# Kernel tuning notes

Hardware: AMD Instinct MI355X
Metric: run time of the kernel (lower is better)

## Reference

```python
import jax, jax.numpy as jnp
import numpy as np

B, C_IN, L = 16, 64, 1024
HID, OUT, ORDER = 1024, 512, 4
EPS = 1e-5


def setup_inputs() -> dict:
    key = jax.random.key(0)
    ks = jax.random.split(key, 4)
    return {
        "x": jax.random.normal(ks[0], (B, C_IN, L), jnp.float32),
        "W_in": jax.random.normal(ks[1], (C_IN, HID), jnp.float32) / np.sqrt(C_IN).astype(np.float32),
        "b_in": jnp.zeros((HID,), jnp.float32),
        "coeffs1": jax.random.normal(ks[2], (HID, HID, ORDER), jnp.float32) * 0.01,
        "bias1": jnp.zeros((HID,), jnp.float32),
        "g1": jnp.ones((HID,), jnp.float32),
        "beta1": jnp.zeros((HID,), jnp.float32),
        "coeffs2": jax.random.normal(ks[3], (OUT, HID, ORDER), jnp.float32) * 0.01,
        "bias2": jnp.zeros((OUT,), jnp.float32),
        "g2": jnp.ones((OUT,), jnp.float32),
        "beta2": jnp.zeros((OUT,), jnp.float32),
    }


def _taylor_kan(x, coeffs, bias):
    # x: (B, L, C_in); coeffs: (out, C_in, order); y[b,l,o] = sum_i sum_c x^i * coeffs[o,c,i]
    # Expressed as order-wise GEMMs with a running power -- no (B,out,L,C) expand.
    order = coeffs.shape[-1]
    y = jnp.zeros(x.shape[:2] + (coeffs.shape[0],), x.dtype)
    xp = jnp.ones_like(x)  # x**0 (matches torch 0**0 == 1)
    for i in range(order):
        y = y + jnp.einsum('blc,oc->blo', xp, coeffs[:, :, i])
        if i + 1 < order:
            xp = xp * x
    return y + bias


def _layernorm(x, g, b):
    mu = jnp.mean(x, -1, keepdims=True)
    var = jnp.mean((x - mu) ** 2, -1, keepdims=True)
    return (x - mu) * jax.lax.rsqrt(var + EPS) * g + b


def reference(x, W_in, b_in, coeffs1, bias1, g1, beta1, coeffs2, bias2, g2, beta2):
    # x: (B, C_in, L) -> project channels to hidden: (B, L, HID)
    h = jnp.einsum('bcl,ch->blh', x, W_in) + b_in
    h = _taylor_kan(h, coeffs1, bias1)            # (B, L, HID)
    h = jax.nn.gelu(_layernorm(h, g1, beta1), approximate=False)
    h = _taylor_kan(h, coeffs2, bias2)            # (B, L, OUT)
    h = _layernorm(h, g2, beta2)
    return jnp.mean(h, axis=1)                    # adaptive avg pool over L -> (B, OUT)
```

## Files before the change

### kernel.cpp

```cpp
#include <hip/hip_runtime.h>
#include <math.h>

#define Bsz  16
#define CIN  64
#define LEN  1024
#define HIDN 1024
#define OUTN 512
#define MTOT (Bsz*LEN)
#define KTOT (3*HIDN)
#define LCHUNKS 32
#define LROWS   (LEN/LCHUNKS)

typedef __attribute__((ext_vector_type(8))) short bf16x8;
typedef __attribute__((ext_vector_type(16))) float f32x16;

__device__ __forceinline__ unsigned short f2bf(float x) {
    union { float f; unsigned int u; } v; v.f = x;
    unsigned int r = v.u + 0x7fff + ((v.u >> 16) & 1);
    return (unsigned short)(r >> 16);
}
__device__ __forceinline__ float bf2f(unsigned short u) {
    union { unsigned int u; float f; } v; v.u = ((unsigned int)u) << 16;
    return v.f;
}
__device__ __forceinline__ void gload_lds16(const void* g, void* l) {
    __builtin_amdgcn_global_load_lds((const __attribute__((address_space(1))) void*)g,
                                     (__attribute__((address_space(3))) void*)l, 16, 0, 0);
}

__global__ __launch_bounds__(256) void prep_all(const float* __restrict__ coeffs1,
                                                const float* __restrict__ bias1,
                                                const float* __restrict__ coeffs2,
                                                const float* __restrict__ bias2,
                                                const float* __restrict__ x,
                                                const float* __restrict__ Win,
                                                unsigned short* __restrict__ W1T,
                                                float* __restrict__ b1e,
                                                unsigned short* __restrict__ W2T,
                                                float* __restrict__ b2e,
                                                unsigned short* __restrict__ xT,
                                                unsigned short* __restrict__ WinT) {
    __shared__ float sm[64 * 65];
    int bid = blockIdx.x, t = threadIdx.x;
    if (bid < 1536) {
        const float* coeffs; const float* bias; unsigned short* WT; float* beff; int o;
        if (bid < 1024) { coeffs = coeffs1; bias = bias1; WT = W1T; beff = b1e; o = bid; }
        else            { coeffs = coeffs2; bias = bias2; WT = W2T; beff = b2e; o = bid - 1024; }
        float s = 0.f;
        unsigned short* wrow = WT + (size_t)o * KTOT;
        for (int c = t; c < HIDN; c += 256) {
            float4 v = *(const float4*)(coeffs + ((size_t)o * HIDN + c) * 4);
            s += v.x;
            wrow[c]            = f2bf(v.y);
            wrow[HIDN + c]     = f2bf(v.z);
            wrow[2 * HIDN + c] = f2bf(v.w);
        }
        for (int off = 32; off > 0; off >>= 1) s += __shfl_down(s, off, 64);
        if ((t & 63) == 0) sm[t >> 6] = s;
        __syncthreads();
        if (t == 0) beff[o] = bias[o] + sm[0] + sm[1] + sm[2] + sm[3];
    } else {
        const float* src; unsigned short* dstbase; size_t src_rstride;
        int c0;
        if (bid < 1792) {
            int tile = bid - 1536; int b = tile >> 4; c0 = (tile & 15) * 64;
            src = x + (size_t)b * CIN * LEN;  src_rstride = LEN;
            dstbase = xT + ((size_t)b * LEN + c0) * CIN;
        } else {
            int tile = bid - 1792; c0 = tile * 64;
            src = Win; src_rstride = HIDN;
            dstbase = WinT + (size_t)c0 * CIN;
        }
#pragma unroll
        for (int it = 0; it < 4; it++) {
            int idx = t + it * 256;
            int c = idx >> 4, q = idx & 15;
            float4 v = *(const float4*)(src + (size_t)c * src_rstride + c0 + q * 4);
            sm[c * 65 + q * 4 + 0] = v.x;
            sm[c * 65 + q * 4 + 1] = v.y;
            sm[c * 65 + q * 4 + 2] = v.z;
            sm[c * 65 + q * 4 + 3] = v.w;
        }
        __syncthreads();
        int ll = t >> 2, cg = (t & 3) * 16;
        unsigned short* dst = dstbase + (size_t)ll * CIN + cg;
#pragma unroll
        for (int j = 0; j < 4; j++) {
            int c = cg + j * 4;
            ushort4 w = { f2bf(sm[(c + 0) * 65 + ll]), f2bf(sm[(c + 1) * 65 + ll]),
                          f2bf(sm[(c + 2) * 65 + ll]), f2bf(sm[(c + 3) * 65 + ll]) };
            *(ushort4*)(dst + j * 4) = w;
        }
    }
}

__global__ __launch_bounds__(256) void proj_mfma(const unsigned short* __restrict__ xT,
                                                 const unsigned short* __restrict__ WinT,
                                                 const float* __restrict__ bin,
                                                 unsigned short* __restrict__ Hpow) {
    __shared__ unsigned short As[128 * 64];
    __shared__ unsigned short Bs[128 * 64];
    int t = threadIdx.x, lane = t & 63, wave = t >> 6;
    int m0 = blockIdx.x * 128, n0 = blockIdx.y * 128;
    int srow = lane >> 3, sgcc = (lane & 7) ^ srow;
    const unsigned short* Ab = xT + (size_t)m0 * CIN;
    const unsigned short* Bb = WinT + (size_t)n0 * CIN;

    f32x16 acc[2][2] = {};
    int wr = (wave >> 1) * 64, wc = (wave & 1) * 64;
    int row32 = lane & 31, half = lane >> 5;

#pragma unroll
    for (int j = 0; j < 4; j++) {
        int rgrp = wave * 32 + j * 8;
        gload_lds16(Ab + (size_t)(rgrp + srow) * CIN + sgcc * 8, As + rgrp * 64);
        gload_lds16(Bb + (size_t)(rgrp + srow) * CIN + sgcc * 8, Bs + rgrp * 64);
    }
    __syncthreads();
#pragma unroll
    for (int ks = 0; ks < 4; ks++) {
        int cidx = ks * 2 + half;
        bf16x8 af[2], bf[2];
#pragma unroll
        for (int mt = 0; mt < 2; mt++) {
            int r = wr + mt * 32 + row32;
            af[mt] = *(const bf16x8*)(As + r * 64 + ((cidx ^ (r & 7)) << 3));
        }
#pragma unroll
        for (int nt = 0; nt < 2; nt++) {
            int c = wc + nt * 32 + row32;
            bf[nt] = *(const bf16x8*)(Bs + c * 64 + ((cidx ^ (c & 7)) << 3));
        }
#pragma unroll
        for (int mt = 0; mt < 2; mt++)
#pragma unroll
            for (int nt = 0; nt < 2; nt++)
                acc[mt][nt] = __builtin_amdgcn_mfma_f32_32x32x16_bf16(af[mt], bf[nt], acc[mt][nt], 0, 0, 0);
    }
#pragma unroll
    for (int nt = 0; nt < 2; nt++) {
        int oc = n0 + wc + nt * 32 + row32;
        float bo = bin[oc];
#pragma unroll
        for (int mt = 0; mt < 2; mt++) {
#pragma unroll
            for (int reg = 0; reg < 16; reg++) {
                int rl = (reg & 3) + 8 * (reg >> 2) + 4 * half;
                size_t mr = (size_t)(m0 + wr + mt * 32 + rl);
                float h = acc[mt][nt][reg] + bo;
                unsigned short* d = Hpow + mr * KTOT + oc;
                d[0]        = f2bf(h);
                d[HIDN]     = f2bf(h * h);
                d[2 * HIDN] = f2bf(h * h * h);
            }
        }
    }
}

template<int N, bool BF16OUT>
__global__ __launch_bounds__(256) void mfma_gemm(const unsigned short* __restrict__ A,
                                                 const unsigned short* __restrict__ BT,
                                                 const float* __restrict__ beff,
                                                 void* __restrict__ Yv) {
    __shared__ unsigned short As[128 * 64];
    __shared__ unsigned short Bs[128 * 64];
    int t = threadIdx.x;
    int lane = t & 63, wave = t >> 6;
    int m0 = blockIdx.x * 128, n0 = blockIdx.y * 128;
    const unsigned short* Ab = A + (size_t)m0 * KTOT;
    const unsigned short* Bb = BT + (size_t)n0 * KTOT;

    int srow = lane >> 3;
    int sgcc = (lane & 7) ^ srow;

    f32x16 acc[2][2] = {};
    int wr = (wave >> 1) * 64;
    int wc = (wave & 1) * 64;
    int row32 = lane & 31, half = lane >> 5;

    for (int k0 = 0; k0 < KTOT; k0 += 64) {
#pragma unroll
        for (int j = 0; j < 4; j++) {
            int rgrp = wave * 32 + j * 8;
            gload_lds16(Ab + ((size_t)(rgrp + srow) * KTOT + k0 + sgcc * 8), As + rgrp * 64);
            gload_lds16(Bb + ((size_t)(rgrp + srow) * KTOT + k0 + sgcc * 8), Bs + rgrp * 64);
        }
        __syncthreads();
#pragma unroll
        for (int ks = 0; ks < 4; ks++) {
            int cidx = ks * 2 + half;
            bf16x8 af[2], bf[2];
#pragma unroll
            for (int mt = 0; mt < 2; mt++) {
                int r = wr + mt * 32 + row32;
                af[mt] = *(const bf16x8*)(As + r * 64 + ((cidx ^ (r & 7)) << 3));
            }
#pragma unroll
            for (int nt = 0; nt < 2; nt++) {
                int c = wc + nt * 32 + row32;
                bf[nt] = *(const bf16x8*)(Bs + c * 64 + ((cidx ^ (c & 7)) << 3));
            }
#pragma unroll
            for (int mt = 0; mt < 2; mt++)
#pragma unroll
                for (int nt = 0; nt < 2; nt++)
                    acc[mt][nt] = __builtin_amdgcn_mfma_f32_32x32x16_bf16(af[mt], bf[nt], acc[mt][nt], 0, 0, 0);
        }
        __syncthreads();
    }
#pragma unroll
    for (int nt = 0; nt < 2; nt++) {
        int oc = n0 + wc + nt * 32 + row32;
        float bo = beff[oc];
#pragma unroll
        for (int mt = 0; mt < 2; mt++) {
#pragma unroll
            for (int reg = 0; reg < 16; reg++) {
                int rl = (reg & 3) + 8 * (reg >> 2) + 4 * half;
                int mr = m0 + wr + mt * 32 + rl;
                float v = acc[mt][nt][reg] + bo;
                if (BF16OUT) ((unsigned short*)Yv)[(size_t)mr * N + oc] = f2bf(v);
                else         ((float*)Yv)[(size_t)mr * N + oc] = v;
            }
        }
    }
}

__global__ __launch_bounds__(256) void ln_gelu(const unsigned short* __restrict__ y1,
                                               const float* __restrict__ g,
                                               const float* __restrict__ be,
                                               unsigned short* __restrict__ Gpow) {
    __shared__ float red[4];
    int m = blockIdx.x, t = threadIdx.x;
    const unsigned short* row = y1 + (size_t)m * HIDN;
    ushort4 u = *(const ushort4*)(row + 4 * t);
    float v[4] = { bf2f(u.x), bf2f(u.y), bf2f(u.z), bf2f(u.w) };
    float s = v[0] + v[1] + v[2] + v[3];
    for (int off = 32; off > 0; off >>= 1) s += __shfl_down(s, off, 64);
    if ((t & 63) == 0) red[t >> 6] = s;
    __syncthreads();
    float mu = (red[0] + red[1] + red[2] + red[3]) * (1.f / HIDN);
    __syncthreads();
    float ss = 0.f;
#pragma unroll
    for (int j = 0; j < 4; j++) { float d = v[j] - mu; ss += d * d; }
    for (int off = 32; off > 0; off >>= 1) ss += __shfl_down(ss, off, 64);
    if ((t & 63) == 0) red[t >> 6] = ss;
    __syncthreads();
    float rs = rsqrtf((red[0] + red[1] + red[2] + red[3]) * (1.f / HIDN) + 1e-5f);
    float4 gg = *(const float4*)(g + 4 * t);
    float4 bb = *(const float4*)(be + 4 * t);
    float gl[4];
    float gv[4] = { gg.x, gg.y, gg.z, gg.w };
    float bv[4] = { bb.x, bb.y, bb.z, bb.w };
#pragma unroll
    for (int j = 0; j < 4; j++) {
        float xn = (v[j] - mu) * rs * gv[j] + bv[j];
        gl[j] = xn * 0.5f * (1.f + erff(xn * 0.70710678118654752f));
    }
    unsigned short* dst = Gpow + (size_t)m * KTOT + 4 * t;
    ushort4 p1 = { f2bf(gl[0]), f2bf(gl[1]), f2bf(gl[2]), f2bf(gl[3]) };
    ushort4 p2 = { f2bf(gl[0]*gl[0]), f2bf(gl[1]*gl[1]), f2bf(gl[2]*gl[2]), f2bf(gl[3]*gl[3]) };
    ushort4 p3 = { f2bf(gl[0]*gl[0]*gl[0]), f2bf(gl[1]*gl[1]*gl[1]),
                   f2bf(gl[2]*gl[2]*gl[2]), f2bf(gl[3]*gl[3]*gl[3]) };
    *(ushort4*)(dst)          = p1;
    *(ushort4*)(dst + HIDN)   = p2;
    *(ushort4*)(dst + 2*HIDN) = p3;
}

__global__ __launch_bounds__(256) void ln_pool_partial(const float* __restrict__ y2,
                                                       const float* __restrict__ g,
                                                       const float* __restrict__ be,
                                                       float* __restrict__ partial) {
    __shared__ float part[4][OUTN];
    int t = threadIdx.x, lane = t & 63, wave = t >> 6;
    int b = blockIdx.x, chunk = blockIdx.y;
    int mbase = b * LEN + chunk * LROWS;

    float4 gg0 = *(const float4*)(g + 4 * lane);
    float4 gg1 = *(const float4*)(g + 256 + 4 * lane);
    float4 bb0 = *(const float4*)(be + 4 * lane);
    float4 bb1 = *(const float4*)(be + 256 + 4 * lane);

    float acc[8] = {0.f, 0.f, 0.f, 0.f, 0.f, 0.f, 0.f, 0.f};
    for (int rr = wave; rr < LROWS; rr += 4) {
        const float* row = y2 + (size_t)(mbase + rr) * OUTN;
        float4 v0 = *(const float4*)(row + 4 * lane);
        float4 v1 = *(const float4*)(row + 256 + 4 * lane);
        float s  = v0.x + v0.y + v0.z + v0.w + v1.x + v1.y + v1.z + v1.w;
        float ss = v0.x*v0.x + v0.y*v0.y + v0.z*v0.z + v0.w*v0.w
                 + v1.x*v1.x + v1.y*v1.y + v1.z*v1.z + v1.w*v1.w;
        for (int off = 32; off > 0; off >>= 1) {
            s  += __shfl_down(s, off, 64);
            ss += __shfl_down(ss, off, 64);
        }
        s  = __shfl(s, 0, 64);
        ss = __shfl(ss, 0, 64);
        float mu = s * (1.f / OUTN);
        float var = ss * (1.f / OUTN) - mu * mu;
        float rs = rsqrtf(var + 1e-5f);
        acc[0] += (v0.x - mu) * rs * gg0.x + bb0.x;
        acc[1] += (v0.y - mu) * rs * gg0.y + bb0.y;
        acc[2] += (v0.z - mu) * rs * gg0.z + bb0.z;
        acc[3] += (v0.w - mu) * rs * gg0.w + bb0.w;
        acc[4] += (v1.x - mu) * rs * gg1.x + bb1.x;
        acc[5] += (v1.y - mu) * rs * gg1.y + bb1.y;
        acc[6] += (v1.z - mu) * rs * gg1.z + bb1.z;
        acc[7] += (v1.w - mu) * rs * gg1.w + bb1.w;
    }
    *(float4*)(&part[wave][4 * lane])       = *(float4*)(&acc[0]);
    *(float4*)(&part[wave][256 + 4 * lane]) = *(float4*)(&acc[4]);
    __syncthreads();
    float p0 = part[0][2*t] + part[1][2*t] + part[2][2*t] + part[3][2*t];
    float p1 = part[0][2*t+1] + part[1][2*t+1] + part[2][2*t+1] + part[3][2*t+1];
    float* dst = partial + ((size_t)b * LCHUNKS + chunk) * OUTN;
    *(float2*)(dst + 2 * t) = make_float2(p0, p1);
}

__global__ __launch_bounds__(256) void pool_reduce(const float* __restrict__ partial,
                                                   float* __restrict__ out) {
    int b = blockIdx.x, t = threadIdx.x;
    const float* src = partial + (size_t)b * LCHUNKS * OUTN;
    float s0 = 0.f, s1 = 0.f;
    for (int c = 0; c < LCHUNKS; c++) {
        float2 v = *(const float2*)(src + (size_t)c * OUTN + 2 * t);
        s0 += v.x; s1 += v.y;
    }
    *(float2*)(out + (size_t)b * OUTN + 2 * t) = make_float2(s0 * (1.f / LEN), s1 * (1.f / LEN));
}

extern "C" void kernel_launch(void* const* d_in, const int* in_sizes, int n_in,
                              void* d_out, int out_size, void* d_ws, size_t ws_size,
                              hipStream_t stream) {
    const float* x       = (const float*)d_in[0];
    const float* Win     = (const float*)d_in[1];
    const float* bin     = (const float*)d_in[2];
    const float* coeffs1 = (const float*)d_in[3];
    const float* bias1   = (const float*)d_in[4];
    const float* g1      = (const float*)d_in[5];
    const float* beta1   = (const float*)d_in[6];
    const float* coeffs2 = (const float*)d_in[7];
    const float* bias2   = (const float*)d_in[8];
    const float* g2      = (const float*)d_in[9];
    const float* beta2   = (const float*)d_in[10];
    float* out = (float*)d_out;

    char* ws = (char*)d_ws;
    unsigned short* Hpow = (unsigned short*)ws;
    char* p1 = ws + (size_t)MTOT * KTOT * 2;
    unsigned short* y1   = (unsigned short*)p1;
    float*          y2   = (float*)p1;
    char* p2 = p1 + (size_t)MTOT * HIDN * 2;
    unsigned short* W1T  = (unsigned short*)p2;
    char* p3 = p2 + (size_t)HIDN * KTOT * 2;
    unsigned short* W2T  = (unsigned short*)p3;
    char* p4 = p3 + (size_t)OUTN * KTOT * 2;
    float* b1e = (float*)p4;
    float* b2e = (float*)(p4 + HIDN * sizeof(float));
    char* p5 = p4 + (HIDN + OUTN) * sizeof(float);
    unsigned short* xT   = (unsigned short*)p5;
    char* p6 = p5 + (size_t)MTOT * CIN * 2;
    unsigned short* WinT = (unsigned short*)p6;
    unsigned short* G2pow = Hpow;
    float* partial = (float*)W1T;

    prep_all<<<1808, 256, 0, stream>>>(coeffs1, bias1, coeffs2, bias2, x, Win,
                                       W1T, b1e, W2T, b2e, xT, WinT);
    proj_mfma<<<dim3(MTOT / 128, HIDN / 128), 256, 0, stream>>>(xT, WinT, bin, Hpow);
    mfma_gemm<HIDN, true><<<dim3(MTOT / 128, HIDN / 128), 256, 0, stream>>>(Hpow, W1T, b1e, y1);
    ln_gelu<<<MTOT, 256, 0, stream>>>(y1, g1, beta1, G2pow);
    mfma_gemm<OUTN, false><<<dim3(MTOT / 128, OUTN / 128), 256, 0, stream>>>(G2pow, W2T, b2e, y2);
    ln_pool_partial<<<dim3(Bsz, LCHUNKS), 256, 0, stream>>>(y2, g2, beta2, partial);
    pool_reduce<<<Bsz, 256, 0, stream>>>(partial, out);
}
```

Measured before the change: 314.5 us.

## Vectorize epilogue stores via LDS staging, pack LN rows, store y2 in bf16

The projection kernel now stages its output tile in shared memory and writes h, h^2 and h^3 as 16-byte vectors instead of scattered 2-byte stores. ln_gelu handles two rows per block with 8 elements per thread and fuses the mean and variance reductions into one pass. The second GEMM writes bf16 instead of fp32, halving y2 traffic, and ln_pool_partial reads it as packed bf16. This trades some precision in y2 and the variance (single-pass E[x^2]-mu^2) for lower memory bandwidth and fewer uncoalesced writes.

New measurement: 313.2 us. About the same (-0.4%).

```diff
diff --git a/kernel.cpp b/kernel.cpp
--- a/kernel.cpp
+++ b/kernel.cpp
@@ -98,8 +98,10 @@
                                                  const unsigned short* __restrict__ WinT,
                                                  const float* __restrict__ bin,
                                                  unsigned short* __restrict__ Hpow) {
-    __shared__ unsigned short As[128 * 64];
-    __shared__ unsigned short Bs[128 * 64];
+    __shared__ unsigned short smem[2 * 128 * 64];
+    unsigned short* As = smem;
+    unsigned short* Bs = smem + 128 * 64;
+    unsigned short* ht = smem;
     int t = threadIdx.x, lane = t & 63, wave = t >> 6;
     int m0 = blockIdx.x * 128, n0 = blockIdx.y * 128;
     int srow = lane >> 3, sgcc = (lane & 7) ^ srow;
@@ -137,23 +139,38 @@
             for (int nt = 0; nt < 2; nt++)
                 acc[mt][nt] = __builtin_amdgcn_mfma_f32_32x32x16_bf16(af[mt], bf[nt], acc[mt][nt], 0, 0, 0);
     }
+    __syncthreads();
 #pragma unroll
     for (int nt = 0; nt < 2; nt++) {
-        int oc = n0 + wc + nt * 32 + row32;
-        float bo = bin[oc];
+        int ocl = wc + nt * 32 + row32;
+        float bo = bin[n0 + ocl];
 #pragma unroll
         for (int mt = 0; mt < 2; mt++) {
 #pragma unroll
             for (int reg = 0; reg < 16; reg++) {
-                int rl = (reg & 3) + 8 * (reg >> 2) + 4 * half;
-                size_t mr = (size_t)(m0 + wr + mt * 32 + rl);
-                float h = acc[mt][nt][reg] + bo;
-                unsigned short* d = Hpow + mr * KTOT + oc;
-                d[0]        = f2bf(h);
-                d[HIDN]     = f2bf(h * h);
-                d[2 * HIDN] = f2bf(h * h * h);
+                int rl = wr + mt * 32 + (reg & 3) + 8 * (reg >> 2) + 4 * half;
+                ht[rl * 128 + ocl] = f2bf(acc[mt][nt][reg] + bo);
             }
         }
+    }
+    __syncthreads();
+#pragma unroll
+    for (int p = 0; p < 8; p++) {
+        int r = p * 16 + (t >> 4);
+        int c = (t & 15) * 8;
+        bf16x8 hv = *(const bf16x8*)(ht + r * 128 + c);
+        bf16x8 h2v, h3v;
+#pragma unroll
+        for (int j = 0; j < 8; j++) {
+            float f = bf2f((unsigned short)hv[j]);
+            float f2 = f * f;
+            h2v[j] = (short)f2bf(f2);
+            h3v[j] = (short)f2bf(f2 * f);
+        }
+        unsigned short* d = Hpow + (size_t)(m0 + r) * KTOT + n0 + c;
+        *(bf16x8*)(d)            = hv;
+        *(bf16x8*)(d + HIDN)     = h2v;
+        *(bf16x8*)(d + 2 * HIDN) = h3v;
     }
 }
 
@@ -230,45 +247,50 @@
                                                const float* __restrict__ g,
                                                const float* __restrict__ be,
                                                unsigned short* __restrict__ Gpow) {
-    __shared__ float red[4];
-    int m = blockIdx.x, t = threadIdx.x;
-    const unsigned short* row = y1 + (size_t)m * HIDN;
-    ushort4 u = *(const ushort4*)(row + 4 * t);
-    float v[4] = { bf2f(u.x), bf2f(u.y), bf2f(u.z), bf2f(u.w) };
-    float s = v[0] + v[1] + v[2] + v[3];
-    for (int off = 32; off > 0; off >>= 1) s += __shfl_down(s, off, 64);
-    if ((t & 63) == 0) red[t >> 6] = s;
-    __syncthreads();
-    float mu = (red[0] + red[1] + red[2] + red[3]) * (1.f / HIDN);
-    __syncthreads();
-    float ss = 0.f;
-#pragma unroll
-    for (int j = 0; j < 4; j++) { float d = v[j] - mu; ss += d * d; }
-    for (int off = 32; off > 0; off >>= 1) ss += __shfl_down(ss, off, 64);
-    if ((t & 63) == 0) red[t >> 6] = ss;
-    __syncthreads();
-    float rs = rsqrtf((red[0] + red[1] + red[2] + red[3]) * (1.f / HIDN) + 1e-5f);
-    float4 gg = *(const float4*)(g + 4 * t);
-    float4 bb = *(const float4*)(be + 4 * t);
-    float gl[4];
-    float gv[4] = { gg.x, gg.y, gg.z, gg.w };
-    float bv[4] = { bb.x, bb.y, bb.z, bb.w };
-#pragma unroll
-    for (int j = 0; j < 4; j++) {
+    __shared__ float2 red[2][2];
+    int t = threadIdx.x;
+    int rhalf = t >> 7, l = t & 127, wid = (t >> 6) & 1;
+    int m = blockIdx.x * 2 + rhalf;
+    bf16x8 u = *(const bf16x8*)(y1 + (size_t)m * HIDN + l * 8);
+    float v[8];
+    float s = 0.f, ss = 0.f;
+#pragma unroll
+    for (int j = 0; j < 8; j++) {
+        v[j] = bf2f((unsigned short)u[j]);
+        s += v[j]; ss += v[j] * v[j];
+    }
+    for (int off = 32; off > 0; off >>= 1) {
+        s  += __shfl_down(s, off, 64);
+        ss += __shfl_down(ss, off, 64);
+    }
+    if ((t & 63) == 0) red[rhalf][wid] = make_float2(s, ss);
+    __syncthreads();
+    float sT  = red[rhalf][0].x + red[rhalf][1].x;
+    float ssT = red[rhalf][0].y + red[rhalf][1].y;
+    float mu = sT * (1.f / HIDN);
+    float var = ssT * (1.f / HIDN) - mu * mu;
+    float rs = rsqrtf(var + 1e-5f);
+    float4 gA = *(const float4*)(g + l * 8),  gB = *(const float4*)(g + l * 8 + 4);
+    float4 bA = *(const float4*)(be + l * 8), bB = *(const float4*)(be + l * 8 + 4);
+    float gv[8] = { gA.x, gA.y, gA.z, gA.w, gB.x, gB.y, gB.z, gB.w };
+    float bv[8] = { bA.x, bA.y, bA.z, bA.w, bB.x, bB.y, bB.z, bB.w };
+    bf16x8 p1, p2, p3;
+#pragma unroll
+    for (int j = 0; j < 8; j++) {
         float xn = (v[j] - mu) * rs * gv[j] + bv[j];
-        gl[j] = xn * 0.5f * (1.f + erff(xn * 0.70710678118654752f));
-    }
-    unsigned short* dst = Gpow + (size_t)m * KTOT + 4 * t;
-    ushort4 p1 = { f2bf(gl[0]), f2bf(gl[1]), f2bf(gl[2]), f2bf(gl[3]) };
-    ushort4 p2 = { f2bf(gl[0]*gl[0]), f2bf(gl[1]*gl[1]), f2bf(gl[2]*gl[2]), f2bf(gl[3]*gl[3]) };
-    ushort4 p3 = { f2bf(gl[0]*gl[0]*gl[0]), f2bf(gl[1]*gl[1]*gl[1]),
-                   f2bf(gl[2]*gl[2]*gl[2]), f2bf(gl[3]*gl[3]*gl[3]) };
-    *(ushort4*)(dst)          = p1;
-    *(ushort4*)(dst + HIDN)   = p2;
-    *(ushort4*)(dst + 2*HIDN) = p3;
-}
-
-__global__ __launch_bounds__(256) void ln_pool_partial(const float* __restrict__ y2,
+        float gl = xn * 0.5f * (1.f + erff(xn * 0.70710678118654752f));
+        float g2 = gl * gl;
+        p1[j] = (short)f2bf(gl);
+        p2[j] = (short)f2bf(g2);
+        p3[j] = (short)f2bf(g2 * gl);
+    }
+    unsigned short* dst = Gpow + (size_t)m * KTOT + l * 8;
+    *(bf16x8*)(dst)            = p1;
+    *(bf16x8*)(dst + HIDN)     = p2;
+    *(bf16x8*)(dst + 2 * HIDN) = p3;
+}
+
+__global__ __launch_bounds__(256) void ln_pool_partial(const unsigned short* __restrict__ y2,
                                                        const float* __restrict__ g,
                                                        const float* __restrict__ be,
                                                        float* __restrict__ partial) {
@@ -277,19 +299,21 @@
     int b = blockIdx.x, chunk = blockIdx.y;
     int mbase = b * LEN + chunk * LROWS;
 
-    float4 gg0 = *(const float4*)(g + 4 * lane);
-    float4 gg1 = *(const float4*)(g + 256 + 4 * lane);
-    float4 bb0 = *(const float4*)(be + 4 * lane);
-    float4 bb1 = *(const float4*)(be + 256 + 4 * lane);
+    float4 gA = *(const float4*)(g + 8 * lane),  gB = *(const float4*)(g + 8 * lane + 4);
+    float4 bA = *(const float4*)(be + 8 * lane), bB = *(const float4*)(be + 8 * lane + 4);
+    float gv[8] = { gA.x, gA.y, gA.z, gA.w, gB.x, gB.y, gB.z, gB.w };
+    float bv[8] = { bA.x, bA.y, bA.z, bA.w, bB.x, bB.y, bB.z, bB.w };
 
     float acc[8] = {0.f, 0.f, 0.f, 0.f, 0.f, 0.f, 0.f, 0.f};
     for (int rr = wave; rr < LROWS; rr += 4) {
-        const float* row = y2 + (size_t)(mbase + rr) * OUTN;
-        float4 v0 = *(const float4*)(row + 4 * lane);
-        float4 v1 = *(const float4*)(row + 256 + 4 * lane);
-        float s  = v0.x + v0.y + v0.z + v0.w + v1.x + v1.y + v1.z + v1.w;
-        float ss = v0.x*v0.x + v0.y*v0.y + v0.z*v0.z + v0.w*v0.w
-                 + v1.x*v1.x + v1.y*v1.y + v1.z*v1.z + v1.w*v1.w;
+        bf16x8 u = *(const bf16x8*)(y2 + (size_t)(mbase + rr) * OUTN + 8 * lane);
+        float v[8];
+        float s = 0.f, ss = 0.f;
+#pragma unroll
+        for (int j = 0; j < 8; j++) {
+            v[j] = bf2f((unsigned short)u[j]);
+            s += v[j]; ss += v[j] * v[j];
+        }
         for (int off = 32; off > 0; off >>= 1) {
             s  += __shfl_down(s, off, 64);
             ss += __shfl_down(ss, off, 64);
@@ -299,17 +323,12 @@
         float mu = s * (1.f / OUTN);
         float var = ss * (1.f / OUTN) - mu * mu;
         float rs = rsqrtf(var + 1e-5f);
-        acc[0] += (v0.x - mu) * rs * gg0.x + bb0.x;
-        acc[1] += (v0.y - mu) * rs * gg0.y + bb0.y;
-        acc[2] += (v0.z - mu) * rs * gg0.z + bb0.z;
-        acc[3] += (v0.w - mu) * rs * gg0.w + bb0.w;
-        acc[4] += (v1.x - mu) * rs * gg1.x + bb1.x;
-        acc[5] += (v1.y - mu) * rs * gg1.y + bb1.y;
-        acc[6] += (v1.z - mu) * rs * gg1.z + bb1.z;
-        acc[7] += (v1.w - mu) * rs * gg1.w + bb1.w;
-    }
-    *(float4*)(&part[wave][4 * lane])       = *(float4*)(&acc[0]);
-    *(float4*)(&part[wave][256 + 4 * lane]) = *(float4*)(&acc[4]);
+#pragma unroll
+        for (int j = 0; j < 8; j++)
+            acc[j] += (v[j] - mu) * rs * gv[j] + bv[j];
+    }
+    *(float4*)(&part[wave][8 * lane])     = *(float4*)(&acc[0]);
+    *(float4*)(&part[wave][8 * lane + 4]) = *(float4*)(&acc[4]);
     __syncthreads();
     float p0 = part[0][2*t] + part[1][2*t] + part[2][2*t] + part[3][2*t];
     float p1 = part[0][2*t+1] + part[1][2*t+1] + part[2][2*t+1] + part[3][2*t+1];
@@ -349,7 +368,7 @@
     unsigned short* Hpow = (unsigned short*)ws;
     char* p1 = ws + (size_t)MTOT * KTOT * 2;
     unsigned short* y1   = (unsigned short*)p1;
-    float*          y2   = (float*)p1;
+    unsigned short* y2   = (unsigned short*)p1;
     char* p2 = p1 + (size_t)MTOT * HIDN * 2;
     unsigned short* W1T  = (unsigned short*)p2;
     char* p3 = p2 + (size_t)HIDN * KTOT * 2;
@@ -368,8 +387,8 @@
                                        W1T, b1e, W2T, b2e, xT, WinT);
     proj_mfma<<<dim3(MTOT / 128, HIDN / 128), 256, 0, stream>>>(xT, WinT, bin, Hpow);
     mfma_gemm<HIDN, true><<<dim3(MTOT / 128, HIDN / 128), 256, 0, stream>>>(Hpow, W1T, b1e, y1);
-    ln_gelu<<<MTOT, 256, 0, stream>>>(y1, g1, beta1, G2pow);
-    mfma_gemm<OUTN, false><<<dim3(MTOT / 128, OUTN / 128), 256, 0, stream>>>(G2pow, W2T, b2e, y2);
+    ln_gelu<<<MTOT / 2, 256, 0, stream>>>(y1, g1, beta1, G2pow);
+    mfma_gemm<OUTN, true><<<dim3(MTOT / 128, OUTN / 128), 256, 0, stream>>>(G2pow, W2T, b2e, y2);
     ln_pool_partial<<<dim3(Bsz, LCHUNKS), 256, 0, stream>>>(y2, g2, beta2, partial);
     pool_reduce<<<Bsz, 256, 0, stream>>>(partial, out);
 }
```
